# Performance work log

Hardware: AMD Instinct MI355X
Metric: run time of the kernel (lower is better)

The kernel has to match this reference:

```python
import jax, jax.numpy as jnp
import numpy as np
import math

B, C, H, W = 64, 32, 80, 80
HEADS, HD = 8, 4
L = H * W
INV_PI = 1.0 / math.pi


def _conv2d(x, w, pad):
    return jax.lax.conv_general_dilated(x, w, (1, 1), pad, dimension_numbers=('NCHW', 'OIHW', 'NCHW'))


def _lin_angular(x, qkv_w, proj_w, proj_b, dconv_w):
    # x: (B, L, C) -> softmax-free angular linear attention
    qkv = (x @ qkv_w.T).reshape(B, L, 3, HEADS, HD).transpose(2, 0, 3, 1, 4)
    q, k, v = qkv[0], qkv[1], qkv[2]  # (B, HEADS, L, HD)
    q = q / jnp.linalg.norm(q, axis=-1, keepdims=True)
    k = k / jnp.linalg.norm(k, axis=-1, keepdims=True)
    # depthwise conv over L with kernel (9,1), one channel per head
    dconv_v = jax.lax.conv_general_dilated(v, dconv_w, (1, 1), ((4, 4), (0, 0)),
                                           feature_group_count=HEADS,
                                           dimension_numbers=('NCHW', 'OIHW', 'NCHW'))
    attn = jnp.einsum('bhld,bhle->bhde', k, v)  # (B,H,HD,HD)
    out = 0.5 * v + INV_PI * jnp.einsum('bhld,bhde->bhle', q, attn)
    out = out / jnp.linalg.norm(out, axis=-1, keepdims=True)
    out = out + dconv_v
    out = out.transpose(0, 2, 1, 3).reshape(B, L, C)
    return out @ proj_w.T + proj_b


def _xca(x, qkv_w, temp, proj_w, proj_b):
    # x: (B, L, C) -> cross-covariance (channel) attention
    qkv = (x @ qkv_w.T).reshape(B, L, 3, HEADS, HD).transpose(2, 0, 3, 4, 1)
    q, k, v = qkv[0], qkv[1], qkv[2]  # (B, HEADS, HD, L)
    q = q / jnp.maximum(jnp.linalg.norm(q, axis=-1, keepdims=True), 1e-12)
    k = k / jnp.maximum(jnp.linalg.norm(k, axis=-1, keepdims=True), 1e-12)
    attn = jax.nn.softmax(jnp.einsum('bhdn,bhen->bhde', q, k) * temp, axis=-1)
    out = jnp.einsum('bhde,bhen->bhdn', attn, v)  # (B,H,HD,L)
    out = out.transpose(0, 3, 1, 2).reshape(B, L, C)
    return out @ proj_w.T + proj_b


def _chan_vec(f, wa, ba, wa2, ba2, wm, bm, wm2, bm2):
    # f: (B, C, L) -> (B, C, 1) pooled channel descriptor (avg + max branches)
    avg = f.mean(axis=-1)  # (B, C)
    mx = f.max(axis=-1)    # (B, C)
    a = jax.nn.relu(avg @ wa.T + ba) @ wa2.T + ba2
    m = jax.nn.relu(mx @ wm.T + bm) @ wm2.T + bm2
    return (a + m)[..., None]  # (B, C, 1)


def _spatial_gate(a, c1w, c1b, c2w, c2b):
    # a: (B, C, L) -> (B, 1, L) softmax spatial gate
    am = a.reshape(B, C, H, W)
    pooled = jnp.concatenate([am.mean(axis=1, keepdims=True), am.max(axis=1, keepdims=True)], axis=1)
    y = jax.nn.relu(_conv2d(pooled, c1w, ((1, 1), (1, 1))) + c1b[None, :, None, None])
    y = _conv2d(y, c2w, ((1, 1), (1, 1))) + c2b[None, :, None, None]
    return jax.nn.softmax(y.reshape(B, 1, L), axis=-1)


def _forward(rgb, freq, la_qkv_w, la_proj_w, la_proj_b, la_dconv_w,
             xa_qkv_w, xa_temp, xa_proj_w, xa_proj_b,
             c1s_w, c1s_b, c2s_w, c2s_b,
             avg1_w, avg1_b, max1_w, max1_b, avg2_w, avg2_b, max2_w, max2_b,
             avg11_w, avg11_b, max11_w, max11_b, avg22_w, avg22_b, max22_w, max22_b):
    x1 = rgb.reshape(B, C, L).transpose(0, 2, 1)  # to_3d: (B, L, C)
    la1 = _lin_angular(x1, la_qkv_w, la_proj_w, la_proj_b, la_dconv_w)
    x2 = freq.reshape(B, C, L).transpose(0, 2, 1)
    xa1 = _xca(x2, xa_qkv_w, xa_temp, xa_proj_w, xa_proj_b)
    # CAFM works on flattened (B, C, L)
    f1 = la1.transpose(0, 2, 1)
    f2 = xa1.transpose(0, 2, 1)
    a1 = _chan_vec(f1, avg1_w, avg1_b, avg11_w, avg11_b, max1_w, max1_b, max11_w, max11_b)
    a2 = _chan_vec(f2, avg2_w, avg2_b, avg22_w, avg22_b, max2_w, max2_b, max22_w, max22_b)
    cross = jnp.einsum('bci,bdi->bcd', a1, a2)  # (B, C, C)
    a1f = jnp.einsum('bcd,bdl->bcl', jax.nn.softmax(cross, axis=-1), f1)
    a2f = jnp.einsum('bcd,bdl->bcl', jax.nn.softmax(cross.transpose(0, 2, 1), axis=-1), f2)
    g1 = _spatial_gate(a1f, c1s_w, c1s_b, c2s_w, c2s_b)
    g2 = _spatial_gate(a2f, c1s_w, c1s_b, c2s_w, c2s_b)
    f1 = f1 * g1 + f1
    f2 = f2 * g2 + f2
    # torch: (B,C,L).transpose(0,1) -> (C,B,L); sum; permute(1,2,0) -> (B,L,C); to_4d -> (B,C,H,W)
    # transposes cancel: equivalent to (f1+f2).reshape(B, C, H, W)
    return (f1 + f2).reshape(B, C, H, W)


def setup_inputs() -> dict:
    key = jax.random.key(0)
    ks = iter(jax.random.split(key, 40))
    def rn(shape, s=0.05):
        return jax.random.normal(next(ks), shape, dtype=jnp.float32) * s
    return dict(
        rgb=jax.random.normal(next(ks), (B, C, H, W), dtype=jnp.float32),
        freq=jax.random.normal(next(ks), (B, C, H, W), dtype=jnp.float32),
        la_qkv_w=rn((3 * C, C)), la_proj_w=rn((C, C)), la_proj_b=jnp.zeros((C,), jnp.float32),
        la_dconv_w=rn((HEADS, 1, 9, 1)),
        xa_qkv_w=rn((3 * C, C)), xa_temp=jnp.ones((HEADS, 1, 1), jnp.float32),
        xa_proj_w=rn((C, C)), xa_proj_b=jnp.zeros((C,), jnp.float32),
        c1s_w=rn((1, 2, 3, 3)), c1s_b=jnp.zeros((1,), jnp.float32),
        c2s_w=rn((1, 1, 3, 3)), c2s_b=jnp.zeros((1,), jnp.float32),
        avg1_w=rn((16, C)), avg1_b=jnp.zeros((16,), jnp.float32),
        max1_w=rn((16, C)), max1_b=jnp.zeros((16,), jnp.float32),
        avg2_w=rn((16, C)), avg2_b=jnp.zeros((16,), jnp.float32),
        max2_w=rn((16, C)), max2_b=jnp.zeros((16,), jnp.float32),
        avg11_w=rn((C, 16)), avg11_b=jnp.zeros((C,), jnp.float32),
        max11_w=rn((C, 16)), max11_b=jnp.zeros((C,), jnp.float32),
        avg22_w=rn((C, 16)), avg22_b=jnp.zeros((C,), jnp.float32),
        max22_w=rn((C, 16)), max22_b=jnp.zeros((C,), jnp.float32),
    )


def reference(rgb, freq, la_qkv_w, la_proj_w, la_proj_b, la_dconv_w,
              xa_qkv_w, xa_temp, xa_proj_w, xa_proj_b,
              c1s_w, c1s_b, c2s_w, c2s_b,
              avg1_w, avg1_b, max1_w, max1_b, avg2_w, avg2_b, max2_w, max2_b,
              avg11_w, avg11_b, max11_w, max11_b, avg22_w, avg22_b, max22_w, max22_b):
    return _forward(rgb, freq, la_qkv_w, la_proj_w, la_proj_b, la_dconv_w,
                    xa_qkv_w, xa_temp, xa_proj_w, xa_proj_b,
                    c1s_w, c1s_b, c2s_w, c2s_b,
                    avg1_w, avg1_b, max1_w, max1_b, avg2_w, avg2_b, max2_w, max2_b,
                    avg11_w, avg11_b, max11_w, max11_b, avg22_w, avg22_b, max22_w, max22_b)
```

## Files before the change

kernel.cpp:

```cpp
#include <hip/hip_runtime.h>

#define BN 64
#define CN 32
#define HEADSN 8
#define HDN 4
#define LN 6400
#define CL (CN*LN)


__device__ __forceinline__ unsigned fenc(float f){
  unsigned u = __float_as_uint(f);
  return (u & 0x80000000u) ? ~u : (u | 0x80000000u);
}
__device__ __forceinline__ float fdec(unsigned u){
  unsigned v = (u & 0x80000000u) ? (u & 0x7FFFFFFFu) : ~u;
  return __uint_as_float(v);
}

__device__ __forceinline__ unsigned pk_bf16(float a, float b){
  unsigned ua = __float_as_uint(a), ub = __float_as_uint(b);
  ua = (ua + 0x7fffu + ((ua >> 16) & 1u)) >> 16;
  ub = (ub + 0x7fffu + ((ub >> 16) & 1u)) >> 16;
  return ua | (ub << 16);
}
__device__ __forceinline__ float2 upk_bf16(unsigned u){
  return make_float2(__uint_as_float(u << 16), __uint_as_float(u & 0xffff0000u));
}

template<bool MAXOP>
__device__ __forceinline__ float bfly32(const float* in, int lane, int* chOut){
  const bool h0 = (lane & 1)  != 0, h1 = (lane & 2)  != 0, h2 = (lane & 4) != 0,
             h3 = (lane & 8)  != 0, h4 = (lane & 16) != 0;
  float a[16];
  #pragma unroll
  for (int i = 0; i < 16; ++i){
    float send = h0 ? in[i] : in[i+16];
    float keep = h0 ? in[i+16] : in[i];
    float recv = __shfl_xor(send, 1, 64);
    a[i] = MAXOP ? fmaxf(keep, recv) : keep + recv;
  }
  float b[8];
  #pragma unroll
  for (int i = 0; i < 8; ++i){
    float send = h1 ? a[i] : a[i+8];
    float keep = h1 ? a[i+8] : a[i];
    float recv = __shfl_xor(send, 2, 64);
    b[i] = MAXOP ? fmaxf(keep, recv) : keep + recv;
  }
  float c[4];
  #pragma unroll
  for (int i = 0; i < 4; ++i){
    float send = h2 ? b[i] : b[i+4];
    float keep = h2 ? b[i+4] : b[i];
    float recv = __shfl_xor(send, 4, 64);
    c[i] = MAXOP ? fmaxf(keep, recv) : keep + recv;
  }
  float d[2];
  #pragma unroll
  for (int i = 0; i < 2; ++i){
    float send = h3 ? c[i] : c[i+2];
    float keep = h3 ? c[i+2] : c[i];
    float recv = __shfl_xor(send, 8, 64);
    d[i] = MAXOP ? fmaxf(keep, recv) : keep + recv;
  }
  float e;
  {
    float send = h4 ? d[0] : d[1];
    float keep = h4 ? d[1] : d[0];
    float recv = __shfl_xor(send, 16, 64);
    e = MAXOP ? fmaxf(keep, recv) : keep + recv;
  }
  {
    float recv = __shfl_xor(e, 32, 64);
    e = MAXOP ? fmaxf(e, recv) : e + recv;
  }
  *chOut = (h0?16:0)|(h1?8:0)|(h2?4:0)|(h3?2:0)|(h4?1:0);
  return e;
}

__device__ __forceinline__ float bfly16_sum(const float* in, int lane, int* chOut){
  const bool h0 = (lane & 1) != 0, h1 = (lane & 2) != 0, h2 = (lane & 4) != 0,
             h3 = (lane & 8) != 0;
  float a[8];
  #pragma unroll
  for (int i = 0; i < 8; ++i){
    float send = h0 ? in[i] : in[i+8];
    float keep = h0 ? in[i+8] : in[i];
    float recv = __shfl_xor(send, 1, 64);
    a[i] = keep + recv;
  }
  float b[4];
  #pragma unroll
  for (int i = 0; i < 4; ++i){
    float send = h1 ? a[i] : a[i+4];
    float keep = h1 ? a[i+4] : a[i];
    float recv = __shfl_xor(send, 2, 64);
    b[i] = keep + recv;
  }
  float c[2];
  #pragma unroll
  for (int i = 0; i < 2; ++i){
    float send = h2 ? b[i] : b[i+2];
    float keep = h2 ? b[i+2] : b[i];
    float recv = __shfl_xor(send, 4, 64);
    c[i] = keep + recv;
  }
  float e;
  {
    float send = h3 ? c[0] : c[1];
    float keep = h3 ? c[1] : c[0];
    float recv = __shfl_xor(send, 8, 64);
    e = keep + recv;
  }
  e += __shfl_xor(e, 16, 64);
  e += __shfl_xor(e, 32, 64);
  *chOut = (h0?8:0)|(h1?4:0)|(h2?2:0)|(h3?1:0);
  return e;
}

__global__ __launch_bounds__(512) void k_reduce2(const float* __restrict__ rgb,
    const float* __restrict__ freq, const float* __restrict__ Wla,
    const float* __restrict__ Wxa, float* __restrict__ la_attn,
    float* __restrict__ xa_sums){
  __shared__ float2 xs2[2*128*17];
  const bool isXA = blockIdx.x >= 25;
  const int b = blockIdx.y, tid = threadIdx.x;
  const int half = tid >> 8;
  const int wt = tid & 255;
  const int bxt = isXA ? (int)blockIdx.x - 25 : (int)blockIdx.x;
  const int l0 = (bxt*2 + half)*128;
  const float* xg = (isXA ? freq : rgb) + (size_t)b*CL + l0;
  float2* xs = xs2 + half*(128*17);
  {
    const int px = wt & 127;
    const int c2b_ = (wt >> 7)*8;
    #pragma unroll
    for (int j = 0; j < 8; ++j){
      const int c2 = c2b_ + j;
      float e0 = xg[(2*c2)*LN + px];
      float e1 = xg[(2*c2+1)*LN + px];
      xs[px*17 + c2] = make_float2(e0, e1);
    }
  }
  __syncthreads();
  const int wave = __builtin_amdgcn_readfirstlane((tid >> 6) & 3);
  const int lane = tid & 63;
  if (!isXA){
    const float* Wk = Wla + (32 + wave*8)*32;
    const float* Wv = Wla + (64 + wave*8)*32;
    float acc[32];
    #pragma unroll
    for (int i = 0; i < 32; ++i) acc[i] = 0.f;
    for (int it = 0; it < 2; ++it){
      const int ll = it*64 + lane;
      float xv[32];
      #pragma unroll
      for (int c2 = 0; c2 < 16; ++c2){
        float2 t = xs[ll*17 + c2];
        xv[2*c2] = t.x; xv[2*c2+1] = t.y;
      }
      float kk[8], vv[8];
      #pragma unroll
      for (int r = 0; r < 8; ++r){ kk[r] = 0.f; vv[r] = 0.f; }
      #pragma unroll
      for (int c = 0; c < 32; ++c){
        #pragma unroll
        for (int r = 0; r < 8; ++r){
          kk[r] = fmaf(Wk[r*32 + c], xv[c], kk[r]);
          vv[r] = fmaf(Wv[r*32 + c], xv[c], vv[r]);
        }
      }
      #pragma unroll
      for (int hh = 0; hh < 2; ++hh){
        const float* k = kk + hh*4;
        const float* v = vv + hh*4;
        float rn = rsqrtf(k[0]*k[0] + k[1]*k[1] + k[2]*k[2] + k[3]*k[3]);
        #pragma unroll
        for (int d = 0; d < 4; ++d){
          float kn = k[d]*rn;
          #pragma unroll
          for (int e = 0; e < 4; ++e)
            acc[hh*16 + d*4 + e] = fmaf(kn, v[e], acc[hh*16 + d*4 + e]);
        }
      }
    }
    int ch;
    float s = bfly32<false>(acc, lane, &ch);
    if (lane < 32) atomicAdd(la_attn + b*128 + wave*32 + ch, s);
  } else {
    const float* Wq = Wxa + (0  + wave*8)*32;
    const float* Wk = Wxa + (32 + wave*8)*32;
    float acc[48];
    #pragma unroll
    for (int i = 0; i < 48; ++i) acc[i] = 0.f;
    for (int it = 0; it < 2; ++it){
      const int ll = it*64 + lane;
      float xv[32];
      #pragma unroll
      for (int c2 = 0; c2 < 16; ++c2){
        float2 t = xs[ll*17 + c2];
        xv[2*c2] = t.x; xv[2*c2+1] = t.y;
      }
      float qq[8], kk[8];
      #pragma unroll
      for (int r = 0; r < 8; ++r){ qq[r] = 0.f; kk[r] = 0.f; }
      #pragma unroll
      for (int c = 0; c < 32; ++c){
        #pragma unroll
        for (int r = 0; r < 8; ++r){
          qq[r] = fmaf(Wq[r*32 + c], xv[c], qq[r]);
          kk[r] = fmaf(Wk[r*32 + c], xv[c], kk[r]);
        }
      }
      #pragma unroll
      for (int hh = 0; hh < 2; ++hh){
        const float* q = qq + hh*4;
        const float* k = kk + hh*4;
        const int base = hh*24;
        #pragma unroll
        for (int d = 0; d < 4; ++d){
          #pragma unroll
          for (int e = 0; e < 4; ++e)
            acc[base + d*4 + e] = fmaf(q[d], k[e], acc[base + d*4 + e]);
        }
        #pragma unroll
        for (int d = 0; d < 4; ++d) acc[base + 16 + d] = fmaf(q[d], q[d], acc[base + 16 + d]);
        #pragma unroll
        for (int e = 0; e < 4; ++e) acc[base + 20 + e] = fmaf(k[e], k[e], acc[base + 20 + e]);
      }
    }
    float* dst = xa_sums + b*192 + wave*48;
    int ch;
    float s0 = bfly32<false>(acc, lane, &ch);
    if (lane < 32) atomicAdd(dst + ch, s0);
    int ch2;
    float s1 = bfly16_sum(acc + 32, lane, &ch2);
    if (lane < 16) atomicAdd(dst + 32 + ch2, s1);
  }
}

__global__ __launch_bounds__(256) void k_finalize2(const float* __restrict__ rgb,
    const float* __restrict__ freq, const float* __restrict__ Wqkv,
    const float* __restrict__ la_attn, const float* __restrict__ dconv_w,
    const float* __restrict__ Wp, const float* __restrict__ bp,
    const float* __restrict__ Wxa, const float* __restrict__ xtemp,
    const float* __restrict__ xWp, const float* __restrict__ xbp,
    const float* __restrict__ xa_sums,
    float* __restrict__ f1, float* __restrict__ sum1, unsigned* __restrict__ max1e,
    float* __restrict__ f2, float* __restrict__ sum2, unsigned* __restrict__ max2e){
  __shared__ unsigned vsh[264*17];
  __shared__ float M2s[1024];
  __shared__ float attn_s[128];
  const int b = blockIdx.y, l0 = blockIdx.x*256, tid = threadIdx.x;
  const int l = l0 + tid, lane = tid & 63;
  const float* xg = rgb + (size_t)b*CL;
  float x[32];
  #pragma unroll
  for (int c = 0; c < 32; ++c) x[c] = xg[c*LN + l];
  {
    float v[32];
    #pragma unroll
    for (int r = 0; r < 32; ++r) v[r] = 0.f;
    const float* Wv = Wqkv + 64*32;
    #pragma unroll
    for (int c = 0; c < 32; ++c){
      #pragma unroll
      for (int r = 0; r < 32; ++r) v[r] = fmaf(Wv[r*32 + c], x[c], v[r]);
    }
    #pragma unroll
    for (int c2 = 0; c2 < 16; ++c2)
      vsh[(tid+4)*17 + c2] = pk_bf16(v[2*c2], v[2*c2+1]);
  }
  if (tid < 128){
    const int p = tid >> 4, c2 = tid & 15;
    const int hl  = (p < 4) ? (l0 - 4 + p) : (l0 + 252 + p);
    const int pos = (p < 4) ? p : (256 + p);
    float2 vh = make_float2(0.f, 0.f);
    if (hl >= 0 && hl < LN){
      const float* W0 = Wqkv + (64 + 2*c2)*32;
      #pragma unroll 8
      for (int cc = 0; cc < 32; ++cc){
        float xv = xg[cc*LN + hl];
        vh.x = fmaf(W0[cc],      xv, vh.x);
        vh.y = fmaf(W0[32 + cc], xv, vh.y);
      }
    }
    vsh[pos*17 + c2] = pk_bf16(vh.x, vh.y);
  }
  if (tid < 32){
    const int h = tid >> 2, d = tid & 3;
    const float* xss = xa_sums + b*192 + h*24;
    const float tmp = xtemp[h];
    const float nq = fmaxf(sqrtf(xss[16 + d]), 1e-12f);
    float lg[4]; float m = -1e30f;
    #pragma unroll
    for (int e = 0; e < 4; ++e){
      float nk = fmaxf(sqrtf(xss[20 + e]), 1e-12f);
      lg[e] = xss[d*4 + e] * tmp / (nq*nk);
      m = fmaxf(m, lg[e]);
    }
    float Z = 0.f;
    #pragma unroll
    for (int e = 0; e < 4; ++e){ lg[e] = __expf(lg[e] - m); Z += lg[e]; }
    float iZ = 1.f/Z;
    #pragma unroll
    for (int e = 0; e < 4; ++e) attn_s[h*16 + d*4 + e] = lg[e]*iZ;
  }
  __syncthreads();
  if (tid < 32){
    const int c = tid;
    const float* Wv = Wxa + 64*32;
    float tmpv[32];
    #pragma unroll
    for (int k = 0; k < 32; ++k){
      const int h = k >> 2, d = k & 3;
      float s = 0.f;
      #pragma unroll
      for (int e = 0; e < 4; ++e)
        s = fmaf(attn_s[h*16 + d*4 + e], Wv[(h*4 + e)*32 + c], s);
      tmpv[k] = s;
    }
    float out[32];
    #pragma unroll
    for (int r = 0; r < 32; ++r) out[r] = 0.f;
    #pragma unroll
    for (int k = 0; k < 32; ++k){
      #pragma unroll
      for (int r = 0; r < 32; ++r)
        out[r] = fmaf(xWp[r*32 + k], tmpv[k], out[r]);
    }
    #pragma unroll
    for (int r = 0; r < 32; ++r) M2s[r*32 + c] = out[r];
  }
  {
    float y[32];
    #pragma unroll
    for (int h = 0; h < 8; ++h){
      float q0 = 0.f, q1 = 0.f, q2 = 0.f, q3 = 0.f;
      const float* Wq = Wqkv + h*4*32;
      #pragma unroll
      for (int c = 0; c < 32; ++c){
        q0 = fmaf(Wq[c],      x[c], q0);
        q1 = fmaf(Wq[32 + c], x[c], q1);
        q2 = fmaf(Wq[64 + c], x[c], q2);
        q3 = fmaf(Wq[96 + c], x[c], q3);
      }
      const float rnq = rsqrtf(q0*q0 + q1*q1 + q2*q2 + q3*q3);
      q0 *= rnq; q1 *= rnq; q2 *= rnq; q3 *= rnq;
      const float* at = la_attn + b*128 + h*16;
      const float2 v01 = upk_bf16(vsh[(tid+4)*17 + h*2]);
      const float2 v23 = upk_bf16(vsh[(tid+4)*17 + h*2 + 1]);
      const float vo[4] = {v01.x, v01.y, v23.x, v23.y};
      float o[4]; float ss = 0.f;
      #pragma unroll
      for (int e = 0; e < 4; ++e){
        float t = 0.f;
        t = fmaf(q0, at[e],      t);
        t = fmaf(q1, at[4 + e],  t);
        t = fmaf(q2, at[8 + e],  t);
        t = fmaf(q3, at[12 + e], t);
        o[e] = fmaf(0.31830988618379067f, t, 0.5f*vo[e]);
        ss = fmaf(o[e], o[e], ss);
      }
      const float rno = rsqrtf(ss);
      float dc[4] = {0.f, 0.f, 0.f, 0.f};
      #pragma unroll
      for (int j = 0; j < 9; ++j){
        const float w = dconv_w[h*9 + j];
        const float2 p0 = upk_bf16(vsh[(tid + j)*17 + h*2]);
        const float2 p1 = upk_bf16(vsh[(tid + j)*17 + h*2 + 1]);
        dc[0] = fmaf(w, p0.x, dc[0]);
        dc[1] = fmaf(w, p0.y, dc[1]);
        dc[2] = fmaf(w, p1.x, dc[2]);
        dc[3] = fmaf(w, p1.y, dc[3]);
      }
      #pragma unroll
      for (int e = 0; e < 4; ++e) y[h*4 + e] = fmaf(o[e], rno, dc[e]);
    }
    float vals[32];
    float* f1p = f1 + (size_t)b*CL + l;
    #pragma unroll
    for (int r = 0; r < 32; ++r){
      float val = bp[r];
      #pragma unroll
      for (int c = 0; c < 32; ++c) val = fmaf(Wp[r*32 + c], y[c], val);
      f1p[r*LN] = val;
      vals[r] = val;
    }
    int ch;
    float s = bfly32<false>(vals, lane, &ch);
    float m = bfly32<true >(vals, lane, &ch);
    if (lane < 32){
      atomicAdd(&sum1[b*32 + ch], s);
      atomicMax(&max1e[b*32 + ch], fenc(m));
    }
  }
  __syncthreads();
  {
    const float* xf = freq + (size_t)b*CL;
    float xv[32];
    #pragma unroll
    for (int c = 0; c < 32; ++c) xv[c] = xf[c*LN + l];
    float vals[32];
    #pragma unroll
    for (int r = 0; r < 32; ++r) vals[r] = xbp[r];
    #pragma unroll
    for (int c = 0; c < 32; ++c){
      #pragma unroll
      for (int r = 0; r < 32; ++r) vals[r] = fmaf(M2s[r*32 + c], xv[c], vals[r]);
    }
    float* f2p = f2 + (size_t)b*CL + l;
    #pragma unroll
    for (int r = 0; r < 32; ++r) f2p[r*LN] = vals[r];
    int ch;
    float s = bfly32<false>(vals, lane, &ch);
    float m = bfly32<true >(vals, lane, &ch);
    if (lane < 32){
      atomicAdd(&sum2[b*32 + ch], s);
      atomicMax(&max2e[b*32 + ch], fenc(m));
    }
  }
}

__global__ __launch_bounds__(256) void k_mix(const float* __restrict__ f1,
    const float* __restrict__ f2,
    const float* __restrict__ sum1, const unsigned* __restrict__ max1e,
    const float* __restrict__ sum2, const unsigned* __restrict__ max2e,
    const float* __restrict__ a1w, const float* __restrict__ a1b,
    const float* __restrict__ m1w, const float* __restrict__ m1b,
    const float* __restrict__ a2w, const float* __restrict__ a2b,
    const float* __restrict__ m2w, const float* __restrict__ m2b,
    const float* __restrict__ a11w, const float* __restrict__ a11b,
    const float* __restrict__ m11w, const float* __restrict__ m11b,
    const float* __restrict__ a22w, const float* __restrict__ a22b,
    const float* __restrict__ m22w, const float* __restrict__ m22b,
    float* __restrict__ pooled1, float* __restrict__ pooled2){
  __shared__ float avg1[32], mx1[32], avg2[32], mx2[32];
  __shared__ float h_a1[16], h_m1[16], h_a2[16], h_m2[16];
  __shared__ float a1v[32], a2v[32];
  __shared__ float w1s[1024], w2s[1024];
  const int b = blockIdx.y, tid = threadIdx.x;
  const int l = blockIdx.x*256 + tid;
  if (tid < 32){
    avg1[tid] = sum1[b*32 + tid] * (1.f/6400.f);
    mx1[tid]  = fdec(max1e[b*32 + tid]);
    avg2[tid] = sum2[b*32 + tid] * (1.f/6400.f);
    mx2[tid]  = fdec(max2e[b*32 + tid]);
  }
  __syncthreads();
  if (tid < 16){
    float s1 = a1b[tid], s2 = m1b[tid], s3 = a2b[tid], s4 = m2b[tid];
    for (int c = 0; c < 32; ++c){
      s1 = fmaf(avg1[c], a1w[tid*32 + c], s1);
      s2 = fmaf(mx1[c],  m1w[tid*32 + c], s2);
      s3 = fmaf(avg2[c], a2w[tid*32 + c], s3);
      s4 = fmaf(mx2[c],  m2w[tid*32 + c], s4);
    }
    h_a1[tid] = fmaxf(s1, 0.f); h_m1[tid] = fmaxf(s2, 0.f);
    h_a2[tid] = fmaxf(s3, 0.f); h_m2[tid] = fmaxf(s4, 0.f);
  }
  __syncthreads();
  if (tid < 32){
    float v1 = a11b[tid] + m11b[tid];
    float v2 = a22b[tid] + m22b[tid];
    for (int k = 0; k < 16; ++k){
      v1 += h_a1[k]*a11w[tid*16 + k] + h_m1[k]*m11w[tid*16 + k];
      v2 += h_a2[k]*a22w[tid*16 + k] + h_m2[k]*m22w[tid*16 + k];
    }
    a1v[tid] = v1; a2v[tid] = v2;
  }
  __syncthreads();
  if (tid < 32){
    float s = a1v[tid], m = -1e30f;
    for (int d = 0; d < 32; ++d) m = fmaxf(m, s*a2v[d]);
    float Z = 0.f;
    for (int d = 0; d < 32; ++d) Z += __expf(s*a2v[d] - m);
    float iZ = 1.f/Z;
    for (int d = 0; d < 32; ++d) w1s[tid*32 + d] = __expf(s*a2v[d] - m)*iZ;
    float s2 = a2v[tid]; m = -1e30f;
    for (int d = 0; d < 32; ++d) m = fmaxf(m, s2*a1v[d]);
    Z = 0.f;
    for (int d = 0; d < 32; ++d) Z += __expf(s2*a1v[d] - m);
    iZ = 1.f/Z;
    for (int d = 0; d < 32; ++d) w2s[tid*32 + d] = __expf(s2*a1v[d] - m)*iZ;
  }
  __syncthreads();
  float fv[32], av[32];
  {
    const float* f1p = f1 + (size_t)b*CL + l;
    #pragma unroll
    for (int d = 0; d < 32; ++d) fv[d] = f1p[d*LN];
    #pragma unroll
    for (int c = 0; c < 32; ++c) av[c] = 0.f;
    #pragma unroll
    for (int d = 0; d < 32; ++d){
      #pragma unroll
      for (int c = 0; c < 32; ++c) av[c] = fmaf(w1s[c*32 + d], fv[d], av[c]);
    }
    float s = 0.f, m = -1e30f;
    #pragma unroll
    for (int c = 0; c < 32; ++c){ s += av[c]; m = fmaxf(m, av[c]); }
    pooled1[(size_t)b*2*LN + l]      = s*(1.f/32.f);
    pooled1[(size_t)b*2*LN + LN + l] = m;
  }
  {
    const float* f2p = f2 + (size_t)b*CL + l;
    #pragma unroll
    for (int d = 0; d < 32; ++d) fv[d] = f2p[d*LN];
    #pragma unroll
    for (int c = 0; c < 32; ++c) av[c] = 0.f;
    #pragma unroll
    for (int d = 0; d < 32; ++d){
      #pragma unroll
      for (int c = 0; c < 32; ++c) av[c] = fmaf(w2s[c*32 + d], fv[d], av[c]);
    }
    float s = 0.f, m = -1e30f;
    #pragma unroll
    for (int c = 0; c < 32; ++c){ s += av[c]; m = fmaxf(m, av[c]); }
    pooled2[(size_t)b*2*LN + l]      = s*(1.f/32.f);
    pooled2[(size_t)b*2*LN + LN + l] = m;
  }
}

__global__ __launch_bounds__(256) void k_gate(const float* __restrict__ pooled1,
    const float* __restrict__ pooled2, const float* __restrict__ c1w,
    const float* __restrict__ c1b, const float* __restrict__ c2w,
    const float* __restrict__ c2b, float* __restrict__ g1, float* __restrict__ g2){
  __shared__ float y1s[6400];
  __shared__ float red[8];
  const int b = blockIdx.y, t = blockIdx.x, tid = threadIdx.x;
  const float* src = (t == 0 ? pooled1 : pooled2) + (size_t)b*2*LN;
  float* dst = (t == 0 ? g1 : g2) + (size_t)b*LN;
  for (int i = tid; i < 6400; i += 256){
    const int yy = i/80, xx = i - yy*80;
    float a = c1b[0];
    #pragma unroll
    for (int ky = 0; ky < 3; ++ky){
      const int y2 = yy + ky - 1;
      if (y2 < 0 || y2 >= 80) continue;
      #pragma unroll
      for (int kx = 0; kx < 3; ++kx){
        const int x2 = xx + kx - 1;
        if (x2 < 0 || x2 >= 80) continue;
        const int j = y2*80 + x2;
        a = fmaf(src[j],        c1w[ky*3 + kx],     a);
        a = fmaf(src[6400 + j], c1w[9 + ky*3 + kx], a);
      }
    }
    y1s[i] = fmaxf(a, 0.f);
  }
  __syncthreads();
  float y2r[25]; float lmax = -1e30f;
  #pragma unroll
  for (int ii = 0; ii < 25; ++ii){
    const int i = tid + ii*256;
    const int yy = i/80, xx = i - yy*80;
    float a = c2b[0];
    #pragma unroll
    for (int ky = 0; ky < 3; ++ky){
      const int y2 = yy + ky - 1;
      if (y2 < 0 || y2 >= 80) continue;
      #pragma unroll
      for (int kx = 0; kx < 3; ++kx){
        const int x2 = xx + kx - 1;
        if (x2 < 0 || x2 >= 80) continue;
        a = fmaf(y1s[y2*80 + x2], c2w[ky*3 + kx], a);
      }
    }
    y2r[ii] = a; lmax = fmaxf(lmax, a);
  }
  #pragma unroll
  for (int off = 32; off >= 1; off >>= 1) lmax = fmaxf(lmax, __shfl_xor(lmax, off, 64));
  if ((tid & 63) == 0) red[tid >> 6] = lmax;
  __syncthreads();
  const float bmax = fmaxf(fmaxf(red[0], red[1]), fmaxf(red[2], red[3]));
  float lsum = 0.f;
  #pragma unroll
  for (int ii = 0; ii < 25; ++ii){
    float e = __expf(y2r[ii] - bmax);
    y2r[ii] = e; lsum += e;
  }
  #pragma unroll
  for (int off = 32; off >= 1; off >>= 1) lsum += __shfl_xor(lsum, off, 64);
  if ((tid & 63) == 0) red[4 + (tid >> 6)] = lsum;
  __syncthreads();
  const float inv = 1.f/(red[4] + red[5] + red[6] + red[7]);
  #pragma unroll
  for (int ii = 0; ii < 25; ++ii) dst[tid + ii*256] = y2r[ii]*inv;
}

__global__ __launch_bounds__(256) void k_final(const float* __restrict__ f1,
    const float* __restrict__ f2, const float* __restrict__ g1,
    const float* __restrict__ g2, float* __restrict__ out){
  const int i = blockIdx.x*256 + threadIdx.x;
  const int flat = i*4;
  const int b = flat / CL;
  const int rem = flat - b*CL;
  const int l = rem % LN;
  const float4 a  = *(const float4*)(f1 + flat);
  const float4 c  = *(const float4*)(f2 + flat);
  const float4 ga = *(const float4*)(g1 + b*LN + l);
  const float4 gc = *(const float4*)(g2 + b*LN + l);
  float4 o;
  o.x = fmaf(a.x, ga.x, a.x) + fmaf(c.x, gc.x, c.x);
  o.y = fmaf(a.y, ga.y, a.y) + fmaf(c.y, gc.y, c.y);
  o.z = fmaf(a.z, ga.z, a.z) + fmaf(c.z, gc.z, c.z);
  o.w = fmaf(a.w, ga.w, a.w) + fmaf(c.w, gc.w, c.w);
  *(float4*)(out + flat) = o;
}

extern "C" void kernel_launch(void* const* d_in, const int* in_sizes, int n_in,
                              void* d_out, int out_size, void* d_ws, size_t ws_size,
                              hipStream_t stream){
  const float* rgb     = (const float*)d_in[0];
  const float* freq    = (const float*)d_in[1];
  const float* la_qkv  = (const float*)d_in[2];
  const float* la_pw   = (const float*)d_in[3];
  const float* la_pb   = (const float*)d_in[4];
  const float* la_dw   = (const float*)d_in[5];
  const float* xa_qkv  = (const float*)d_in[6];
  const float* xa_temp = (const float*)d_in[7];
  const float* xa_pw   = (const float*)d_in[8];
  const float* xa_pb   = (const float*)d_in[9];
  const float* c1w     = (const float*)d_in[10];
  const float* c1b     = (const float*)d_in[11];
  const float* c2w     = (const float*)d_in[12];
  const float* c2b     = (const float*)d_in[13];

  float* ws = (float*)d_ws;
  size_t o = 0;
  float* f1      = ws + o; o += (size_t)BN*CL;
  float* f2      = ws + o; o += (size_t)BN*CL;
  float* la_attn = ws + o; o += BN*128;
  float* xa_sums = ws + o; o += BN*192;
  float* sum1    = ws + o; o += BN*32;
  unsigned* max1e = (unsigned*)(ws + o); o += BN*32;
  float* sum2    = ws + o; o += BN*32;
  unsigned* max2e = (unsigned*)(ws + o); o += BN*32;
  float* pooled1 = ws + o; o += (size_t)BN*2*LN;
  float* pooled2 = ws + o; o += (size_t)BN*2*LN;
  float* g1      = ws + o; o += (size_t)BN*LN;
  float* g2      = ws + o; o += (size_t)BN*LN;

  const size_t nz = (size_t)BN*128 + BN*192 + (size_t)BN*32*4;
  hipMemsetAsync(la_attn, 0, nz*sizeof(float), stream);

  k_reduce2  <<<dim3(50, BN), 512, 0, stream>>>(rgb, freq, la_qkv, xa_qkv, la_attn, xa_sums);
  k_finalize2<<<dim3(25, BN), 256, 0, stream>>>(rgb, freq, la_qkv, la_attn, la_dw,
                                                la_pw, la_pb,
                                                xa_qkv, xa_temp, xa_pw, xa_pb, xa_sums,
                                                f1, sum1, max1e, f2, sum2, max2e);
  k_mix  <<<dim3(25, BN), 256, 0, stream>>>(f1, f2, sum1, max1e, sum2, max2e,
      (const float*)d_in[14], (const float*)d_in[15], (const float*)d_in[16], (const float*)d_in[17],
      (const float*)d_in[18], (const float*)d_in[19], (const float*)d_in[20], (const float*)d_in[21],
      (const float*)d_in[22], (const float*)d_in[23], (const float*)d_in[24], (const float*)d_in[25],
      (const float*)d_in[26], (const float*)d_in[27], (const float*)d_in[28], (const float*)d_in[29],
      pooled1, pooled2);
  k_gate <<<dim3(2, BN), 256, 0, stream>>>(pooled1, pooled2, c1w, c1b, c2w, c2b, g1, g2);
  k_final<<<12800, 256, 0, stream>>>(f1, f2, g1, g2, (float*)d_out);
}
```

Baseline: 566.2 us.

## Split finalize into separate LA and XCA blocks; widen gate kernel blocks

The finalize kernel's grid doubles so that half the blocks compute the linear-angular branch (f1) and the other half the cross-covariance branch (f2). Previously each block did both in sequence, with 32 threads building the 32x32 mixing matrix serially. That matrix build is now spread across all 256 threads in two shared-memory stages, and register pressure per block drops. Separately, the spatial gate kernel moves from 256 to 1024 threads per block, since it only launches 128 blocks. The costs are redundant per-block mixing-matrix setup and more barriers.

```diff
diff --git a/kernel.cpp b/kernel.cpp
--- a/kernel.cpp
+++ b/kernel.cpp
@@ -249,90 +249,47 @@
     float* __restrict__ f1, float* __restrict__ sum1, unsigned* __restrict__ max1e,
     float* __restrict__ f2, float* __restrict__ sum2, unsigned* __restrict__ max2e){
   __shared__ unsigned vsh[264*17];
-  __shared__ float M2s[1024];
-  __shared__ float attn_s[128];
-  const int b = blockIdx.y, l0 = blockIdx.x*256, tid = threadIdx.x;
+  const bool isXA = blockIdx.x >= 25;
+  const int b = blockIdx.y, tid = threadIdx.x;
+  const int bxt = isXA ? (int)blockIdx.x - 25 : (int)blockIdx.x;
+  const int l0 = bxt*256;
   const int l = l0 + tid, lane = tid & 63;
-  const float* xg = rgb + (size_t)b*CL;
-  float x[32];
-  #pragma unroll
-  for (int c = 0; c < 32; ++c) x[c] = xg[c*LN + l];
-  {
-    float v[32];
-    #pragma unroll
-    for (int r = 0; r < 32; ++r) v[r] = 0.f;
-    const float* Wv = Wqkv + 64*32;
-    #pragma unroll
-    for (int c = 0; c < 32; ++c){
-      #pragma unroll
-      for (int r = 0; r < 32; ++r) v[r] = fmaf(Wv[r*32 + c], x[c], v[r]);
-    }
-    #pragma unroll
-    for (int c2 = 0; c2 < 16; ++c2)
-      vsh[(tid+4)*17 + c2] = pk_bf16(v[2*c2], v[2*c2+1]);
-  }
-  if (tid < 128){
-    const int p = tid >> 4, c2 = tid & 15;
-    const int hl  = (p < 4) ? (l0 - 4 + p) : (l0 + 252 + p);
-    const int pos = (p < 4) ? p : (256 + p);
-    float2 vh = make_float2(0.f, 0.f);
-    if (hl >= 0 && hl < LN){
-      const float* W0 = Wqkv + (64 + 2*c2)*32;
-      #pragma unroll 8
-      for (int cc = 0; cc < 32; ++cc){
-        float xv = xg[cc*LN + hl];
-        vh.x = fmaf(W0[cc],      xv, vh.x);
-        vh.y = fmaf(W0[32 + cc], xv, vh.y);
-      }
-    }
-    vsh[pos*17 + c2] = pk_bf16(vh.x, vh.y);
-  }
-  if (tid < 32){
-    const int h = tid >> 2, d = tid & 3;
-    const float* xss = xa_sums + b*192 + h*24;
-    const float tmp = xtemp[h];
-    const float nq = fmaxf(sqrtf(xss[16 + d]), 1e-12f);
-    float lg[4]; float m = -1e30f;
-    #pragma unroll
-    for (int e = 0; e < 4; ++e){
-      float nk = fmaxf(sqrtf(xss[20 + e]), 1e-12f);
-      lg[e] = xss[d*4 + e] * tmp / (nq*nk);
-      m = fmaxf(m, lg[e]);
-    }
-    float Z = 0.f;
-    #pragma unroll
-    for (int e = 0; e < 4; ++e){ lg[e] = __expf(lg[e] - m); Z += lg[e]; }
-    float iZ = 1.f/Z;
-    #pragma unroll
-    for (int e = 0; e < 4; ++e) attn_s[h*16 + d*4 + e] = lg[e]*iZ;
-  }
-  __syncthreads();
-  if (tid < 32){
-    const int c = tid;
-    const float* Wv = Wxa + 64*32;
-    float tmpv[32];
-    #pragma unroll
-    for (int k = 0; k < 32; ++k){
-      const int h = k >> 2, d = k & 3;
-      float s = 0.f;
-      #pragma unroll
-      for (int e = 0; e < 4; ++e)
-        s = fmaf(attn_s[h*16 + d*4 + e], Wv[(h*4 + e)*32 + c], s);
-      tmpv[k] = s;
-    }
-    float out[32];
-    #pragma unroll
-    for (int r = 0; r < 32; ++r) out[r] = 0.f;
-    #pragma unroll
-    for (int k = 0; k < 32; ++k){
-      #pragma unroll
-      for (int r = 0; r < 32; ++r)
-        out[r] = fmaf(xWp[r*32 + k], tmpv[k], out[r]);
-    }
-    #pragma unroll
-    for (int r = 0; r < 32; ++r) M2s[r*32 + c] = out[r];
-  }
-  {
+  if (!isXA){
+    const float* xg = rgb + (size_t)b*CL;
+    float x[32];
+    #pragma unroll
+    for (int c = 0; c < 32; ++c) x[c] = xg[c*LN + l];
+    {
+      float v[32];
+      #pragma unroll
+      for (int r = 0; r < 32; ++r) v[r] = 0.f;
+      const float* Wv = Wqkv + 64*32;
+      #pragma unroll
+      for (int c = 0; c < 32; ++c){
+        #pragma unroll
+        for (int r = 0; r < 32; ++r) v[r] = fmaf(Wv[r*32 + c], x[c], v[r]);
+      }
+      #pragma unroll
+      for (int c2 = 0; c2 < 16; ++c2)
+        vsh[(tid+4)*17 + c2] = pk_bf16(v[2*c2], v[2*c2+1]);
+    }
+    if (tid < 128){
+      const int p = tid >> 4, c2 = tid & 15;
+      const int hl  = (p < 4) ? (l0 - 4 + p) : (l0 + 252 + p);
+      const int pos = (p < 4) ? p : (256 + p);
+      float2 vh = make_float2(0.f, 0.f);
+      if (hl >= 0 && hl < LN){
+        const float* W0 = Wqkv + (64 + 2*c2)*32;
+        #pragma unroll 8
+        for (int cc = 0; cc < 32; ++cc){
+          float xv = xg[cc*LN + hl];
+          vh.x = fmaf(W0[cc],      xv, vh.x);
+          vh.y = fmaf(W0[32 + cc], xv, vh.y);
+        }
+      }
+      vsh[pos*17 + c2] = pk_bf16(vh.x, vh.y);
+    }
+    __syncthreads();
     float y[32];
     #pragma unroll
     for (int h = 0; h < 8; ++h){
@@ -354,12 +311,12 @@
       float o[4]; float ss = 0.f;
       #pragma unroll
       for (int e = 0; e < 4; ++e){
-        float t = 0.f;
-        t = fmaf(q0, at[e],      t);
-        t = fmaf(q1, at[4 + e],  t);
-        t = fmaf(q2, at[8 + e],  t);
-        t = fmaf(q3, at[12 + e], t);
-        o[e] = fmaf(0.31830988618379067f, t, 0.5f*vo[e]);
+        float tt = 0.f;
+        tt = fmaf(q0, at[e],      tt);
+        tt = fmaf(q1, at[4 + e],  tt);
+        tt = fmaf(q2, at[8 + e],  tt);
+        tt = fmaf(q3, at[12 + e], tt);
+        o[e] = fmaf(0.31830988618379067f, tt, 0.5f*vo[e]);
         ss = fmaf(o[e], o[e], ss);
       }
       const float rno = rsqrtf(ss);
@@ -394,20 +351,69 @@
       atomicAdd(&sum1[b*32 + ch], s);
       atomicMax(&max1e[b*32 + ch], fenc(m));
     }
-  }
-  __syncthreads();
-  {
+  } else {
+    float* attn_s = (float*)vsh;
+    float* tmpv_s = ((float*)vsh) + 128;
+    float* M2s    = ((float*)vsh) + 1152;
     const float* xf = freq + (size_t)b*CL;
-    float xv[32];
-    #pragma unroll
-    for (int c = 0; c < 32; ++c) xv[c] = xf[c*LN + l];
+    float x[32];
+    #pragma unroll
+    for (int c = 0; c < 32; ++c) x[c] = xf[c*LN + l];
+    if (tid < 32){
+      const int h = tid >> 2, d = tid & 3;
+      const float* xss = xa_sums + b*192 + h*24;
+      const float tmp = xtemp[h];
+      const float nq = fmaxf(sqrtf(xss[16 + d]), 1e-12f);
+      float lg[4]; float m = -1e30f;
+      #pragma unroll
+      for (int e = 0; e < 4; ++e){
+        float nk = fmaxf(sqrtf(xss[20 + e]), 1e-12f);
+        lg[e] = xss[d*4 + e] * tmp / (nq*nk);
+        m = fmaxf(m, lg[e]);
+      }
+      float Z = 0.f;
+      #pragma unroll
+      for (int e = 0; e < 4; ++e){ lg[e] = __expf(lg[e] - m); Z += lg[e]; }
+      float iZ = 1.f/Z;
+      #pragma unroll
+      for (int e = 0; e < 4; ++e) attn_s[h*16 + d*4 + e] = lg[e]*iZ;
+    }
+    __syncthreads();
+    {
+      const float* Wv = Wxa + 64*32;
+      #pragma unroll
+      for (int i = 0; i < 4; ++i){
+        const int idx = tid*4 + i;
+        const int k = idx >> 5, c = idx & 31;
+        const int h = k >> 2, d = k & 3;
+        float s = 0.f;
+        #pragma unroll
+        for (int e = 0; e < 4; ++e)
+          s = fmaf(attn_s[h*16 + d*4 + e], Wv[(h*4 + e)*32 + c], s);
+        tmpv_s[k*32 + c] = s;
+      }
+    }
+    __syncthreads();
+    {
+      #pragma unroll
+      for (int i = 0; i < 4; ++i){
+        const int idx = tid*4 + i;
+        const int r = idx >> 5, c = idx & 31;
+        float s = 0.f;
+        #pragma unroll
+        for (int k = 0; k < 32; ++k)
+          s = fmaf(xWp[r*32 + k], tmpv_s[k*32 + c], s);
+        M2s[r*32 + c] = s;
+      }
+    }
+    __syncthreads();
     float vals[32];
     #pragma unroll
     for (int r = 0; r < 32; ++r) vals[r] = xbp[r];
     #pragma unroll
     for (int c = 0; c < 32; ++c){
       #pragma unroll
-      for (int r = 0; r < 32; ++r) vals[r] = fmaf(M2s[r*32 + c], xv[c], vals[r]);
+      for (int r = 0; r < 32; ++r) vals[r] = fmaf(M2s[r*32 + c], x[c], vals[r]);
     }
     float* f2p = f2 + (size_t)b*CL + l;
     #pragma unroll
@@ -522,16 +528,16 @@
   }
 }
 
-__global__ __launch_bounds__(256) void k_gate(const float* __restrict__ pooled1,
+__global__ __launch_bounds__(1024) void k_gate(const float* __restrict__ pooled1,
     const float* __restrict__ pooled2, const float* __restrict__ c1w,
     const float* __restrict__ c1b, const float* __restrict__ c2w,
     const float* __restrict__ c2b, float* __restrict__ g1, float* __restrict__ g2){
   __shared__ float y1s[6400];
-  __shared__ float red[8];
+  __shared__ float red[32];
   const int b = blockIdx.y, t = blockIdx.x, tid = threadIdx.x;
   const float* src = (t == 0 ? pooled1 : pooled2) + (size_t)b*2*LN;
   float* dst = (t == 0 ? g1 : g2) + (size_t)b*LN;
-  for (int i = tid; i < 6400; i += 256){
+  for (int i = tid; i < 6400; i += 1024){
     const int yy = i/80, xx = i - yy*80;
     float a = c1b[0];
     #pragma unroll
@@ -550,43 +556,56 @@
     y1s[i] = fmaxf(a, 0.f);
   }
   __syncthreads();
-  float y2r[25]; float lmax = -1e30f;
-  #pragma unroll
-  for (int ii = 0; ii < 25; ++ii){
-    const int i = tid + ii*256;
-    const int yy = i/80, xx = i - yy*80;
-    float a = c2b[0];
-    #pragma unroll
-    for (int ky = 0; ky < 3; ++ky){
-      const int y2 = yy + ky - 1;
-      if (y2 < 0 || y2 >= 80) continue;
-      #pragma unroll
-      for (int kx = 0; kx < 3; ++kx){
-        const int x2 = xx + kx - 1;
-        if (x2 < 0 || x2 >= 80) continue;
-        a = fmaf(y1s[y2*80 + x2], c2w[ky*3 + kx], a);
-      }
-    }
-    y2r[ii] = a; lmax = fmaxf(lmax, a);
+  float y2r[7]; float lmax = -1e30f;
+  #pragma unroll
+  for (int ii = 0; ii < 7; ++ii){
+    const int i = tid + ii*1024;
+    if (i < 6400){
+      const int yy = i/80, xx = i - yy*80;
+      float a = c2b[0];
+      #pragma unroll
+      for (int ky = 0; ky < 3; ++ky){
+        const int y2 = yy + ky - 1;
+        if (y2 < 0 || y2 >= 80) continue;
+        #pragma unroll
+        for (int kx = 0; kx < 3; ++kx){
+          const int x2 = xx + kx - 1;
+          if (x2 < 0 || x2 >= 80) continue;
+          a = fmaf(y1s[y2*80 + x2], c2w[ky*3 + kx], a);
+        }
+      }
+      y2r[ii] = a; lmax = fmaxf(lmax, a);
+    } else y2r[ii] = -1e30f;
   }
   #pragma unroll
   for (int off = 32; off >= 1; off >>= 1) lmax = fmaxf(lmax, __shfl_xor(lmax, off, 64));
   if ((tid & 63) == 0) red[tid >> 6] = lmax;
   __syncthreads();
-  const float bmax = fmaxf(fmaxf(red[0], red[1]), fmaxf(red[2], red[3]));
+  float bmax = red[0];
+  #pragma unroll
+  for (int i = 1; i < 16; ++i) bmax = fmaxf(bmax, red[i]);
   float lsum = 0.f;
   #pragma unroll
-  for (int ii = 0; ii < 25; ++ii){
-    float e = __expf(y2r[ii] - bmax);
-    y2r[ii] = e; lsum += e;
+  for (int ii = 0; ii < 7; ++ii){
+    const int i = tid + ii*1024;
+    if (i < 6400){
+      float e = __expf(y2r[ii] - bmax);
+      y2r[ii] = e; lsum += e;
+    }
   }
   #pragma unroll
   for (int off = 32; off >= 1; off >>= 1) lsum += __shfl_xor(lsum, off, 64);
-  if ((tid & 63) == 0) red[4 + (tid >> 6)] = lsum;
-  __syncthreads();
-  const float inv = 1.f/(red[4] + red[5] + red[6] + red[7]);
-  #pragma unroll
-  for (int ii = 0; ii < 25; ++ii) dst[tid + ii*256] = y2r[ii]*inv;
+  if ((tid & 63) == 0) red[16 + (tid >> 6)] = lsum;
+  __syncthreads();
+  float tsum = 0.f;
+  #pragma unroll
+  for (int i = 0; i < 16; ++i) tsum += red[16 + i];
+  const float inv = 1.f/tsum;
+  #pragma unroll
+  for (int ii = 0; ii < 7; ++ii){
+    const int i = tid + ii*1024;
+    if (i < 6400) dst[i] = y2r[ii]*inv;
+  }
 }
 
 __global__ __launch_bounds__(256) void k_final(const float* __restrict__ f1,
@@ -646,7 +665,7 @@
   hipMemsetAsync(la_attn, 0, nz*sizeof(float), stream);
 
   k_reduce2  <<<dim3(50, BN), 512, 0, stream>>>(rgb, freq, la_qkv, xa_qkv, la_attn, xa_sums);
-  k_finalize2<<<dim3(25, BN), 256, 0, stream>>>(rgb, freq, la_qkv, la_attn, la_dw,
+  k_finalize2<<<dim3(50, BN), 256, 0, stream>>>(rgb, freq, la_qkv, la_attn, la_dw,
                                                 la_pw, la_pb,
                                                 xa_qkv, xa_temp, xa_pw, xa_pb, xa_sums,
                                                 f1, sum1, max1e, f2, sum2, max2e);
@@ -656,6 +675,6 @@
       (const float*)d_in[22], (const float*)d_in[23], (const float*)d_in[24], (const float*)d_in[25],
       (const float*)d_in[26], (const float*)d_in[27], (const float*)d_in[28], (const float*)d_in[29],
       pooled1, pooled2);
-  k_gate <<<dim3(2, BN), 256, 0, stream>>>(pooled1, pooled2, c1w, c1b, c2w, c2b, g1, g2);
+  k_gate <<<dim3(2, BN), 1024, 0, stream>>>(pooled1, pooled2, c1w, c1b, c2w, c2b, g1, g2);
   k_final<<<12800, 256, 0, stream>>>(f1, f2, g1, g2, (float*)d_out);
 }
```

Result: slower. 584.5 us (+3.2%).
